# Kernel tuning notes

Measured on AMD Instinct MI355X. Metric: run time of the kernel, lower is better.

Reference implementation:

```python
import jax, jax.numpy as jnp
import numpy as np

B, S, D = 1, 2048, 6144
H, KV, HD = 48, 8, 128  # query heads, kv heads, head dim
THETA = 10000.0


def _rope_tables(seq_len, head_dim, theta):
    pos = jnp.arange(seq_len, dtype=jnp.float32)
    inv_freq = 1.0 / (theta ** (jnp.arange(0, head_dim, 2, dtype=jnp.float32) / head_dim))
    freqs = pos[:, None] * inv_freq[None, :]                 # [S, HD/2]
    emb = jnp.concatenate([freqs, freqs], axis=-1)           # [S, HD]
    return jnp.cos(emb), jnp.sin(emb)


def setup_inputs() -> dict:
    key = jax.random.key(0)
    k1, k2, k3 = jax.random.split(key, 3)
    hidden_states = jax.random.normal(k1, (B, S, D), dtype=jnp.float32) * 0.02
    w_qkv = jax.random.normal(k2, (D, (H + 2 * KV) * HD), dtype=jnp.float32) * 0.02
    w_out = jax.random.normal(k3, (H * HD, D), dtype=jnp.float32) * 0.02
    cos, sin = _rope_tables(S, HD, THETA)
    return {"hidden_states": hidden_states, "cos": cos, "sin": sin,
            "w_qkv": w_qkv, "w_out": w_out}


def _rotate_half(x):
    x1, x2 = jnp.split(x, 2, axis=-1)
    return jnp.concatenate([-x2, x1], axis=-1)


def reference(hidden_states, cos, sin, w_qkv, w_out):
    b, s, d = hidden_states.shape
    # fused QKV projection
    qkv = jnp.einsum('bsd,de->bse', hidden_states, w_qkv)
    q = qkv[..., : H * HD].reshape(b, s, H, HD)
    k = qkv[..., H * HD: (H + KV) * HD].reshape(b, s, KV, HD)
    v = qkv[..., (H + KV) * HD:].reshape(b, s, KV, HD)
    # rotary embedding (rotate-half form)
    c = cos[None, :, None, :]
    sn = sin[None, :, None, :]
    q = q * c + _rotate_half(q) * sn
    k = k * c + _rotate_half(k) * sn
    # GQA: expand kv heads to query heads
    rep = H // KV
    k = jnp.repeat(k, rep, axis=2)  # [b, s, H, HD]
    v = jnp.repeat(v, rep, axis=2)
    scale = 1.0 / jnp.sqrt(jnp.float32(HD))
    scores = jnp.einsum('bqhd,bkhd->bhqk', q, k) * scale     # [b,H,S,S]
    causal = jnp.tril(jnp.ones((s, s), dtype=bool))
    scores = jnp.where(causal[None, None], scores, jnp.float32(-1e30))
    attn = jax.nn.softmax(scores, axis=-1)
    out = jnp.einsum('bhqk,bkhd->bqhd', attn, v).reshape(b, s, H * HD)
    return jnp.einsum('bsd,de->bse', out, w_out)
```

## Files before the change

kernel.cpp:

```cpp
#include <hip/hip_runtime.h>


#define S_   2048
#define D_   6144
#define H_   48
#define KV_  8
#define HD_  128
#define NQK  8192
#define REP  6

typedef __attribute__((ext_vector_type(8)))  __bf16 bf16x8;
typedef __attribute__((ext_vector_type(4)))  __bf16 bf16x4;
typedef __attribute__((ext_vector_type(2)))  __bf16 bf16x2;
typedef __attribute__((ext_vector_type(4)))  float  f32x4;
typedef __attribute__((ext_vector_type(16))) float  f32x16;
typedef __attribute__((ext_vector_type(4)))  float  float4v;

__device__ __forceinline__ void gl_lds16(const void* g, void* l) {
  __builtin_amdgcn_global_load_lds(
      (const __attribute__((address_space(1))) void*)g,
      (__attribute__((address_space(3))) void*)l, 16, 0, 0);
}

__device__ __forceinline__ unsigned pack2(float a, float b) {
  union { bf16x2 v; unsigned u; } x;
  x.v[0] = (__bf16)a; x.v[1] = (__bf16)b;
  return x.u;
}

__global__ __launch_bounds__(256) void cvt_bf16(const float* __restrict__ in,
                                                __bf16* __restrict__ out, int n4) {
  int stride = gridDim.x * 256;
  for (int i = blockIdx.x * 256 + threadIdx.x; i < n4; i += stride) {
    float4v v = ((const float4v*)in)[i];
    bf16x4 o;
    o[0] = (__bf16)v[0]; o[1] = (__bf16)v[1];
    o[2] = (__bf16)v[2]; o[3] = (__bf16)v[3];
    ((bf16x4*)out)[i] = o;
  }
}

__global__ __launch_bounds__(256) void wtrans(const float* __restrict__ src,
                                              __bf16* __restrict__ dst,
                                              int K, int N) {
  __shared__ float t[32][33];
  const int n0 = blockIdx.x * 32, k0 = blockIdx.y * 32;
  const int tx = threadIdx.x, ty = threadIdx.y;
#pragma unroll
  for (int r = 0; r < 4; ++r)
    t[ty + r * 8][tx] = src[(size_t)(k0 + ty + r * 8) * N + n0 + tx];
  __syncthreads();
#pragma unroll
  for (int r = 0; r < 4; ++r)
    dst[(size_t)(n0 + ty + r * 8) * K + k0 + tx] = (__bf16)t[tx][ty + r * 8];
}

template <typename CT, int BN>
__global__ __launch_bounds__(512, 2) void gemm_bt(const __bf16* __restrict__ A,
                                                  const __bf16* __restrict__ BT,
                                                  CT* __restrict__ C,
                                                  int M, int N, int K) {
  constexpr int NB = BN / 64;
  constexpr int NF = BN / 64;
  __shared__ __align__(16) __bf16 As[2][256 * 64];
  __shared__ __align__(16) __bf16 Bs[2][BN * 64];
  const int tid = threadIdx.x;
  const int w = tid >> 6, l = tid & 63;
  const int lr = l & 15, lg = l >> 4;
  const int wm = w >> 2, wn = w & 3;
  const int nwg = gridDim.x * gridDim.y;
  int bid = blockIdx.y * gridDim.x + blockIdx.x;
  bid = (bid & 7) * (nwg >> 3) + (bid >> 3);
  const int m0 = (bid / gridDim.x) * 256, n0 = (bid % gridDim.x) * BN;
  const int nkt = K >> 6;

  auto stage_all = [&](int T) {
    const int buf = T & 1, k0 = T << 6;
#pragma unroll
    for (int j = 0; j < 4; ++j) {
      int idx = j * 512 + tid;
      int row = idx >> 3;
      int c = (idx & 7) ^ (row & 7);
      gl_lds16(A + (size_t)(m0 + row) * K + k0 + c * 8,
               As[buf] + (size_t)(j * 512 + w * 64) * 8);
    }
#pragma unroll
    for (int j = 0; j < NB; ++j) {
      int idx = j * 512 + tid;
      int row = idx >> 3;
      int c = (idx & 7) ^ (row & 7);
      gl_lds16(BT + (size_t)(n0 + row) * K + k0 + c * 8,
               Bs[buf] + (size_t)(j * 512 + w * 64) * 8);
    }
  };
  auto rdA = [&](const __bf16* Ab, int mh, int kk, bf16x8* afr) {
#pragma unroll
    for (int m = 0; m < 4; ++m) {
      int row = wm * 128 + (mh * 4 + m) * 16 + lr;
      afr[m] = *(const bf16x8*)(Ab + (size_t)row * 64
                                + (((kk * 4 + lg) ^ (lr & 7)) * 8));
    }
  };
  auto rdB = [&](const __bf16* Bb, int kk, bf16x8* bfr) {
#pragma unroll
    for (int n = 0; n < NF; ++n) {
      int row = wn * (BN / 4) + n * 16 + lr;
      bfr[n] = *(const bf16x8*)(Bb + (size_t)row * 64
                                + (((kk * 4 + lg) ^ (lr & 7)) * 8));
    }
  };
#define SBAR  __builtin_amdgcn_s_barrier()
#define MFMA_CLUSTER(ACC_OFF)                                                   \
  __builtin_amdgcn_s_setprio(1);                                               \
  _Pragma("unroll")                                                             \
  for (int m = 0; m < 4; ++m)                                                   \
    _Pragma("unroll")                                                           \
    for (int n = 0; n < NF; ++n)                                                \
      acc[(ACC_OFF) + m][n] = __builtin_amdgcn_mfma_f32_16x16x32_bf16(          \
          afr[m], bfr[n], acc[(ACC_OFF) + m][n], 0, 0, 0);                      \
  __builtin_amdgcn_s_setprio(0)

  f32x4 acc[8][NF] = {};
  stage_all(0);
  asm volatile("s_waitcnt vmcnt(0)" ::: "memory");
  SBAR;

  for (int T = 0; T < nkt; ++T) {
    const __bf16* Ab = As[T & 1];
    const __bf16* Bb = Bs[T & 1];
    bf16x8 afr[4], bfr[NF];
    rdA(Ab, 0, 0, afr);
    rdB(Bb, 0, bfr);
    if (T + 1 < nkt) stage_all(T + 1);
    MFMA_CLUSTER(0);
    SBAR;
    rdA(Ab, 1, 0, afr);
    MFMA_CLUSTER(4);
    SBAR;
    rdA(Ab, 0, 1, afr);
    rdB(Bb, 1, bfr);
    MFMA_CLUSTER(0);
    SBAR;
    rdA(Ab, 1, 1, afr);
    MFMA_CLUSTER(4);
    asm volatile("s_waitcnt lgkmcnt(0)" ::: "memory");
    if (T + 1 < nkt) asm volatile("s_waitcnt vmcnt(0)" ::: "memory");
    SBAR;
  }
#undef SBAR
#undef MFMA_CLUSTER
#pragma unroll
  for (int m = 0; m < 8; ++m)
#pragma unroll
    for (int n = 0; n < NF; ++n)
#pragma unroll
      for (int j = 0; j < 4; ++j) {
        int row = m0 + wm * 128 + m * 16 + lg * 4 + j;
        int col = n0 + wn * (BN / 4) + n * 16 + lr;
        C[(size_t)row * N + col] = (CT)acc[m][n][j];
      }
}

template <typename CT>
__global__ __launch_bounds__(256, 2) void gemm_bt128(const __bf16* __restrict__ A,
                                                     const __bf16* __restrict__ BT,
                                                     CT* __restrict__ C,
                                                     int M, int N, int K) {
  __shared__ __align__(16) __bf16 As[2][128 * 64];
  __shared__ __align__(16) __bf16 Bs[2][128 * 64];
  const int tid = threadIdx.x;
  const int w = tid >> 6, l = tid & 63;
  const int lr = l & 15, lg = l >> 4;
  const int wm = w >> 1, wn = w & 1;
  const int nwg = gridDim.x * gridDim.y;
  int bid = blockIdx.y * gridDim.x + blockIdx.x;
  bid = (bid & 7) * (nwg >> 3) + (bid >> 3);
  const int m0 = (bid / gridDim.x) * 128, n0 = (bid % gridDim.x) * 128;
  const int nkt = K >> 6;

  auto stage_all = [&](int T) {
    const int buf = T & 1, k0 = T << 6;
#pragma unroll
    for (int j = 0; j < 4; ++j) {
      int idx = j * 256 + tid;
      int row = idx >> 3;
      int c = (idx & 7) ^ (row & 7);
      gl_lds16(A + (size_t)(m0 + row) * K + k0 + c * 8,
               As[buf] + (size_t)(j * 256 + w * 64) * 8);
      gl_lds16(BT + (size_t)(n0 + row) * K + k0 + c * 8,
               Bs[buf] + (size_t)(j * 256 + w * 64) * 8);
    }
  };
  auto rd = [&](const __bf16* Sb, int rbase, int kk, bf16x8* fr) {
#pragma unroll
    for (int m = 0; m < 4; ++m) {
      int row = rbase + m * 16 + lr;
      fr[m] = *(const bf16x8*)(Sb + (size_t)row * 64
                               + (((kk * 4 + lg) ^ (lr & 7)) * 8));
    }
  };

  f32x4 acc[4][4] = {};
  stage_all(0);
  asm volatile("s_waitcnt vmcnt(0)" ::: "memory");
  __builtin_amdgcn_s_barrier();

  for (int T = 0; T < nkt; ++T) {
    const __bf16* Ab = As[T & 1];
    const __bf16* Bb = Bs[T & 1];
    bf16x8 afr[4], bfr[4];
    rd(Ab, wm * 64, 0, afr);
    rd(Bb, wn * 64, 0, bfr);
    if (T + 1 < nkt) stage_all(T + 1);
    __builtin_amdgcn_s_setprio(1);
#pragma unroll
    for (int m = 0; m < 4; ++m)
#pragma unroll
      for (int n = 0; n < 4; ++n)
        acc[m][n] = __builtin_amdgcn_mfma_f32_16x16x32_bf16(afr[m], bfr[n], acc[m][n], 0, 0, 0);
    __builtin_amdgcn_s_setprio(0);
    __builtin_amdgcn_s_barrier();
    rd(Ab, wm * 64, 1, afr);
    rd(Bb, wn * 64, 1, bfr);
    __builtin_amdgcn_s_setprio(1);
#pragma unroll
    for (int m = 0; m < 4; ++m)
#pragma unroll
      for (int n = 0; n < 4; ++n)
        acc[m][n] = __builtin_amdgcn_mfma_f32_16x16x32_bf16(afr[m], bfr[n], acc[m][n], 0, 0, 0);
    __builtin_amdgcn_s_setprio(0);
    asm volatile("s_waitcnt lgkmcnt(0)" ::: "memory");
    if (T + 1 < nkt) asm volatile("s_waitcnt vmcnt(0)" ::: "memory");
    __builtin_amdgcn_s_barrier();
  }
#pragma unroll
  for (int m = 0; m < 4; ++m)
#pragma unroll
    for (int n = 0; n < 4; ++n)
#pragma unroll
      for (int j = 0; j < 4; ++j) {
        int row = m0 + wm * 64 + m * 16 + lg * 4 + j;
        int col = n0 + wn * 64 + n * 16 + lr;
        C[(size_t)row * N + col] = (CT)acc[m][n][j];
      }
}

__global__ __launch_bounds__(256) void rope_qk(const __bf16* __restrict__ qkv,
                                               const float* __restrict__ cosT,
                                               const float* __restrict__ sinT,
                                               __bf16* __restrict__ Qo,
                                               __bf16* __restrict__ Ko) {
  const int s = blockIdx.x;
  const __bf16* base = qkv + (size_t)s * NQK;
  const float* ct = cosT + s * HD_;
  const float* st = sinT + s * HD_;
  const float scale = 0.1275174313f;
  for (int q4 = threadIdx.x; q4 < H_ * HD_ / 4; q4 += 256) {
    int h = q4 >> 5, d = (q4 & 31) * 4;
    bf16x4 x  = *(const bf16x4*)(base + h * HD_ + d);
    bf16x4 xr = (d < 64) ? *(const bf16x4*)(base + h * HD_ + d + 64)
                         : *(const bf16x4*)(base + h * HD_ + d - 64);
    float4v c4 = *(const float4v*)(ct + d);
    float4v s4 = *(const float4v*)(st + d);
    bf16x4 o;
#pragma unroll
    for (int j = 0; j < 4; ++j) {
      float r = (d < 64) ? -(float)xr[j] : (float)xr[j];
      o[j] = (__bf16)(((float)x[j] * c4[j] + r * s4[j]) * scale);
    }
    *(bf16x4*)(Qo + ((size_t)s * H_ + h) * HD_ + d) = o;
  }
  for (int q4 = threadIdx.x; q4 < KV_ * HD_ / 4; q4 += 256) {
    int h = q4 >> 5, d = (q4 & 31) * 4;
    const __bf16* kb = base + H_ * HD_;
    bf16x4 x  = *(const bf16x4*)(kb + h * HD_ + d);
    bf16x4 xr = (d < 64) ? *(const bf16x4*)(kb + h * HD_ + d + 64)
                         : *(const bf16x4*)(kb + h * HD_ + d - 64);
    float4v c4 = *(const float4v*)(ct + d);
    float4v s4 = *(const float4v*)(st + d);
    bf16x4 o;
#pragma unroll
    for (int j = 0; j < 4; ++j) {
      float r = (d < 64) ? -(float)xr[j] : (float)xr[j];
      o[j] = (__bf16)((float)x[j] * c4[j] + r * s4[j]);
    }
    *(bf16x4*)(Ko + ((size_t)s * KV_ + h) * HD_ + d) = o;
  }
}

__global__ __launch_bounds__(256) void v_trans(const __bf16* __restrict__ qkv,
                                               __bf16* __restrict__ Vt) {
  __shared__ __bf16 t[32][36];
  const int s0 = blockIdx.x * 32, d0 = blockIdx.y * 32, h = blockIdx.z;
  const int tx = threadIdx.x, ty = threadIdx.y;
  *(bf16x4*)&t[ty][tx * 4] =
      *(const bf16x4*)(qkv + (size_t)(s0 + ty) * NQK + (H_ + KV_) * HD_ + h * HD_ + d0 + tx * 4);
  __syncthreads();
  bf16x4 o;
#pragma unroll
  for (int j = 0; j < 4; ++j) o[j] = t[tx * 4 + j][ty];
  *(bf16x4*)(Vt + ((size_t)h * HD_ + d0 + ty) * S_ + s0 + tx * 4) = o;
}

__global__ __launch_bounds__(256, 2) void attn(const __bf16* __restrict__ Q,
                                               const __bf16* __restrict__ Kb,
                                               const __bf16* __restrict__ Vt,
                                               __bf16* __restrict__ O) {
  __shared__ __align__(16) __bf16 Ks[2][64 * 128];
  __shared__ __align__(16) __bf16 Vs[2][128 * 64];
  const int bx = gridDim.x - 1 - blockIdx.x;
  const int h = blockIdx.y, kvh = h / REP;
  const int tid = threadIdx.x, w = tid >> 6, l = tid & 63;
  const int c = l & 31, g = l >> 5;
  const int qb = bx * 128;
  const int qrow = qb + w * 32 + c;
  const int tmax_w = (qb + w * 32 + 31) >> 6;
  const int NT = (qb >> 6) + 2;

  auto stage = [&](int t) {
    const int buf = t & 1;
    const int kbase = t << 6;
#pragma unroll
    for (int j = 0; j < 4; ++j) {
      int idx = j * 256 + tid;
      int row = idx >> 4, cc = (idx & 15) ^ (row & 15);
      gl_lds16(Kb + ((size_t)(kbase + row) * KV_ + kvh) * HD_ + cc * 8,
               Ks[buf] + (size_t)(j * 256 + w * 64) * 8);
    }
#pragma unroll
    for (int j = 0; j < 4; ++j) {
      int idx = j * 256 + tid;
      int row = idx >> 3, cc = (idx & 7) ^ (row & 7);
      gl_lds16(Vt + (size_t)(kvh * HD_ + row) * S_ + kbase + cc * 8,
               Vs[buf] + (size_t)(j * 256 + w * 64) * 8);
    }
  };

  bf16x8 qf[8];
  const __bf16* qp = Q + ((size_t)qrow * H_ + h) * HD_ + g * 8;
#pragma unroll
  for (int st = 0; st < 8; ++st) qf[st] = *(const bf16x8*)(qp + st * 16);

  f32x16 o[4] = {};
  float m = -1e30f, lsum = 0.f;

  stage(0);
  __syncthreads();
  for (int t = 0; t < NT; ++t) {
    const int buf = t & 1;
    if (t + 1 < NT) stage(t + 1);
    if (t <= tmax_w) {
      const int kbase = t << 6;
      f32x16 s0 = {}, s1 = {};
      __builtin_amdgcn_s_setprio(1);
#pragma unroll
      for (int st = 0; st < 8; ++st) {
        int ch = ((st * 2 + g) ^ (c & 15)) * 8;
        bf16x8 k0 = *(const bf16x8*)(Ks[buf] + (size_t)c * 128 + ch);
        bf16x8 k1 = *(const bf16x8*)(Ks[buf] + (size_t)(32 + c) * 128 + ch);
        s0 = __builtin_amdgcn_mfma_f32_32x32x16_bf16(k0, qf[st], s0, 0, 0, 0);
        s1 = __builtin_amdgcn_mfma_f32_32x32x16_bf16(k1, qf[st], s1, 0, 0, 0);
      }
      __builtin_amdgcn_s_setprio(0);
      if (t == tmax_w) {
#pragma unroll
        for (int r = 0; r < 16; ++r) {
          int krow = (r & 3) + 8 * (r >> 2) + 4 * g;
          if (kbase + krow > qrow)      s0[r] = -1e30f;
          if (kbase + 32 + krow > qrow) s1[r] = -1e30f;
        }
      }
      float mj = s0[0];
#pragma unroll
      for (int r = 1; r < 16; ++r) mj = fmaxf(mj, s0[r]);
#pragma unroll
      for (int r = 0; r < 16; ++r) mj = fmaxf(mj, s1[r]);
      mj = fmaxf(mj, __shfl_xor(mj, 32));
      if (!__all(mj - m <= 8.0f)) {
        float mnew = fmaxf(m, mj);
        float sc = __builtin_amdgcn_exp2f(m - mnew);
        lsum *= sc;
#pragma unroll
        for (int db = 0; db < 4; ++db)
#pragma unroll
          for (int r = 0; r < 16; ++r) o[db][r] *= sc;
        m = mnew;
      }
      float rs = 0.f;
      float p0[16], p1[16];
#pragma unroll
      for (int r = 0; r < 16; ++r) { p0[r] = __builtin_amdgcn_exp2f(s0[r] - m); rs += p0[r]; }
#pragma unroll
      for (int r = 0; r < 16; ++r) { p1[r] = __builtin_amdgcn_exp2f(s1[r] - m); rs += p1[r]; }
      rs += __shfl_xor(rs, 32);
      lsum += rs;
      unsigned bq[4][4];
#pragma unroll
      for (int n = 0; n < 2; ++n)
#pragma unroll
        for (int tq = 0; tq < 2; ++tq) {
          const float* pp = n ? p1 : p0;
          unsigned q0 = pack2(pp[8 * tq + 0], pp[8 * tq + 1]);
          unsigned q1 = pack2(pp[8 * tq + 2], pp[8 * tq + 3]);
          unsigned q2 = pack2(pp[8 * tq + 4], pp[8 * tq + 5]);
          unsigned q3 = pack2(pp[8 * tq + 6], pp[8 * tq + 7]);
          unsigned v0 = g ? q0 : q2;
          unsigned v1 = g ? q1 : q3;
          unsigned sh0 = (unsigned)__shfl_xor((int)v0, 32);
          unsigned sh1 = (unsigned)__shfl_xor((int)v1, 32);
          int s = n * 2 + tq;
          bq[s][0] = g ? sh0 : q0;
          bq[s][1] = g ? sh1 : q1;
          bq[s][2] = g ? q2 : sh0;
          bq[s][3] = g ? q3 : sh1;
        }
      __builtin_amdgcn_s_setprio(1);
#pragma unroll
      for (int s = 0; s < 4; ++s) {
        union { unsigned u[4]; bf16x8 v; } bb;
        bb.u[0] = bq[s][0]; bb.u[1] = bq[s][1]; bb.u[2] = bq[s][2]; bb.u[3] = bq[s][3];
#pragma unroll
        for (int db = 0; db < 4; ++db) {
          int ch = ((s * 2 + g) ^ (c & 7)) * 8;
          bf16x8 vfr = *(const bf16x8*)(Vs[buf] + (size_t)(db * 32 + c) * 64 + ch);
          o[db] = __builtin_amdgcn_mfma_f32_32x32x16_bf16(vfr, bb.v, o[db], 0, 0, 0);
        }
      }
      __builtin_amdgcn_s_setprio(0);
    }
    if (t + 1 < NT) __syncthreads();
  }
  float inv = 1.f / lsum;
#pragma unroll
  for (int db = 0; db < 4; ++db)
#pragma unroll
    for (int rg = 0; rg < 4; ++rg) {
      bf16x4 ov;
#pragma unroll
      for (int j = 0; j < 4; ++j) ov[j] = (__bf16)(o[db][rg * 4 + j] * inv);
      *(bf16x4*)(O + (size_t)qrow * D_ + h * HD_ + db * 32 + rg * 8 + g * 4) = ov;
    }
}

extern "C" void kernel_launch(void* const* d_in, const int* in_sizes, int n_in,
                              void* d_out, int out_size, void* d_ws, size_t ws_size,
                              hipStream_t stream) {
  const float* hidden = (const float*)d_in[0];
  const float* cosT   = (const float*)d_in[1];
  const float* sinT   = (const float*)d_in[2];
  const float* w_qkv  = (const float*)d_in[3];
  const float* w_out  = (const float*)d_in[4];
  float* out = (float*)d_out;
  char* ws = (char*)d_ws;

  __bf16* wT   = (__bf16*)ws;
  __bf16* hb   = (__bf16*)(ws + 100663296);
  __bf16* qkvb = (__bf16*)(ws + 100663296 + 25165824);
  __bf16* q_b  = (__bf16*)(ws + 100663296 + 25165824 + 33554432);
  __bf16* k_b  = q_b + (size_t)S_ * H_ * HD_;
  __bf16* vt_b = k_b + (size_t)S_ * KV_ * HD_;

  cvt_bf16<<<dim3(2048), dim3(256), 0, stream>>>(hidden, hb, (int)((size_t)S_ * D_ / 4));
  wtrans<<<dim3(NQK / 32, D_ / 32), dim3(32, 8), 0, stream>>>(w_qkv, wT, D_, NQK);
  gemm_bt<__bf16, 256><<<dim3(NQK / 256, S_ / 256), dim3(512), 0, stream>>>(hb, wT, qkvb, S_, NQK, D_);
  rope_qk<<<dim3(S_), dim3(256), 0, stream>>>(qkvb, cosT, sinT, q_b, k_b);
  v_trans<<<dim3(S_ / 32, HD_ / 32, KV_), dim3(8, 32), 0, stream>>>(qkvb, vt_b);
  wtrans<<<dim3(D_ / 32, D_ / 32), dim3(32, 8), 0, stream>>>(w_out, wT, D_, D_);
  attn<<<dim3(S_ / 128, H_), dim3(256), 0, stream>>>(q_b, k_b, vt_b, hb);
  gemm_bt128<float><<<dim3(D_ / 128, S_ / 128), dim3(256), 0, stream>>>(hb, wT, out, S_, D_, D_);
}
```

Measured before the change: 678.7 us.

## Vectorize weight transpose, retile output GEMM to 128x192, simplify attention rescale

The weight transpose kernel now reads float4 rows and writes 8-wide bf16 vectors over 64x32 tiles. This cuts memory transactions in the fp32-to-bf16 weight conversion, which runs every call. The output projection GEMM moves to 512-thread blocks with 128x192 tiles, giving 512 workgroups and more waves per block. The attention kernel drops its lazy conditional rescale for an unconditional online-softmax rescale and no longer reverses block order. That removes the branch but adds 64 multiplies per iteration and may hurt load balance on the causal mask.

```diff
diff --git a/kernel.cpp b/kernel.cpp
--- a/kernel.cpp
+++ b/kernel.cpp
@@ -43,16 +43,24 @@
 __global__ __launch_bounds__(256) void wtrans(const float* __restrict__ src,
                                               __bf16* __restrict__ dst,
                                               int K, int N) {
-  __shared__ float t[32][33];
-  const int n0 = blockIdx.x * 32, k0 = blockIdx.y * 32;
-  const int tx = threadIdx.x, ty = threadIdx.y;
-#pragma unroll
-  for (int r = 0; r < 4; ++r)
-    t[ty + r * 8][tx] = src[(size_t)(k0 + ty + r * 8) * N + n0 + tx];
+  __shared__ float t[64][37];
+  const int n0 = blockIdx.x * 32, k0 = blockIdx.y * 64;
+  const int tid = threadIdx.x;
+  const int kr = tid >> 3, nc = (tid & 7) * 4;
+#pragma unroll
+  for (int i = 0; i < 2; ++i) {
+    float4v v = *(const float4v*)(src + (size_t)(k0 + kr + i * 32) * N + n0 + nc);
+    t[kr + i * 32][nc + 0] = v[0];
+    t[kr + i * 32][nc + 1] = v[1];
+    t[kr + i * 32][nc + 2] = v[2];
+    t[kr + i * 32][nc + 3] = v[3];
+  }
   __syncthreads();
-#pragma unroll
-  for (int r = 0; r < 4; ++r)
-    dst[(size_t)(n0 + ty + r * 8) * K + k0 + tx] = (__bf16)t[tx][ty + r * 8];
+  const int nr = tid >> 3, kc = (tid & 7) * 8;
+  bf16x8 o;
+#pragma unroll
+  for (int j = 0; j < 8; ++j) o[j] = (__bf16)t[kc + j][nr];
+  *(bf16x8*)(dst + (size_t)(n0 + nr) * K + k0 + kc) = o;
 }
 
 template <typename CT, int BN>
@@ -162,45 +170,59 @@
 }
 
 template <typename CT>
-__global__ __launch_bounds__(256, 2) void gemm_bt128(const __bf16* __restrict__ A,
-                                                     const __bf16* __restrict__ BT,
-                                                     CT* __restrict__ C,
-                                                     int M, int N, int K) {
+__global__ __launch_bounds__(512, 2) void gemm2_bt(const __bf16* __restrict__ A,
+                                                   const __bf16* __restrict__ BT,
+                                                   CT* __restrict__ C,
+                                                   int M, int N, int K) {
   __shared__ __align__(16) __bf16 As[2][128 * 64];
-  __shared__ __align__(16) __bf16 Bs[2][128 * 64];
+  __shared__ __align__(16) __bf16 Bs[2][192 * 64];
   const int tid = threadIdx.x;
   const int w = tid >> 6, l = tid & 63;
   const int lr = l & 15, lg = l >> 4;
-  const int wm = w >> 1, wn = w & 1;
+  const int wm = w >> 2, wn = w & 3;
   const int nwg = gridDim.x * gridDim.y;
   int bid = blockIdx.y * gridDim.x + blockIdx.x;
   bid = (bid & 7) * (nwg >> 3) + (bid >> 3);
-  const int m0 = (bid / gridDim.x) * 128, n0 = (bid % gridDim.x) * 128;
+  const int m0 = (bid / gridDim.x) * 128, n0 = (bid % gridDim.x) * 192;
   const int nkt = K >> 6;
 
   auto stage_all = [&](int T) {
     const int buf = T & 1, k0 = T << 6;
 #pragma unroll
-    for (int j = 0; j < 4; ++j) {
-      int idx = j * 256 + tid;
+    for (int j = 0; j < 2; ++j) {
+      int idx = j * 512 + tid;
       int row = idx >> 3;
       int c = (idx & 7) ^ (row & 7);
       gl_lds16(A + (size_t)(m0 + row) * K + k0 + c * 8,
-               As[buf] + (size_t)(j * 256 + w * 64) * 8);
+               As[buf] + (size_t)(j * 512 + w * 64) * 8);
+    }
+#pragma unroll
+    for (int j = 0; j < 3; ++j) {
+      int idx = j * 512 + tid;
+      int row = idx >> 3;
+      int c = (idx & 7) ^ (row & 7);
       gl_lds16(BT + (size_t)(n0 + row) * K + k0 + c * 8,
-               Bs[buf] + (size_t)(j * 256 + w * 64) * 8);
-    }
-  };
-  auto rd = [&](const __bf16* Sb, int rbase, int kk, bf16x8* fr) {
+               Bs[buf] + (size_t)(j * 512 + w * 64) * 8);
+    }
+  };
+  auto rdA = [&](const __bf16* Ab, int kk, bf16x8* afr) {
 #pragma unroll
     for (int m = 0; m < 4; ++m) {
-      int row = rbase + m * 16 + lr;
-      fr[m] = *(const bf16x8*)(Sb + (size_t)row * 64
-                               + (((kk * 4 + lg) ^ (lr & 7)) * 8));
-    }
-  };
-
-  f32x4 acc[4][4] = {};
+      int row = wm * 64 + m * 16 + lr;
+      afr[m] = *(const bf16x8*)(Ab + (size_t)row * 64
+                                + (((kk * 4 + lg) ^ (lr & 7)) * 8));
+    }
+  };
+  auto rdB = [&](const __bf16* Bb, int kk, bf16x8* bfr) {
+#pragma unroll
+    for (int n = 0; n < 3; ++n) {
+      int row = wn * 48 + n * 16 + lr;
+      bfr[n] = *(const bf16x8*)(Bb + (size_t)row * 64
+                                + (((kk * 4 + lg) ^ (lr & 7)) * 8));
+    }
+  };
+
+  f32x4 acc[4][3] = {};
   stage_all(0);
   asm volatile("s_waitcnt vmcnt(0)" ::: "memory");
   __builtin_amdgcn_s_barrier();
@@ -208,25 +230,25 @@
   for (int T = 0; T < nkt; ++T) {
     const __bf16* Ab = As[T & 1];
     const __bf16* Bb = Bs[T & 1];
-    bf16x8 afr[4], bfr[4];
-    rd(Ab, wm * 64, 0, afr);
-    rd(Bb, wn * 64, 0, bfr);
+    bf16x8 afr[4], bfr[3];
+    rdA(Ab, 0, afr);
+    rdB(Bb, 0, bfr);
     if (T + 1 < nkt) stage_all(T + 1);
     __builtin_amdgcn_s_setprio(1);
 #pragma unroll
     for (int m = 0; m < 4; ++m)
 #pragma unroll
-      for (int n = 0; n < 4; ++n)
+      for (int n = 0; n < 3; ++n)
         acc[m][n] = __builtin_amdgcn_mfma_f32_16x16x32_bf16(afr[m], bfr[n], acc[m][n], 0, 0, 0);
     __builtin_amdgcn_s_setprio(0);
     __builtin_amdgcn_s_barrier();
-    rd(Ab, wm * 64, 1, afr);
-    rd(Bb, wn * 64, 1, bfr);
+    rdA(Ab, 1, afr);
+    rdB(Bb, 1, bfr);
     __builtin_amdgcn_s_setprio(1);
 #pragma unroll
     for (int m = 0; m < 4; ++m)
 #pragma unroll
-      for (int n = 0; n < 4; ++n)
+      for (int n = 0; n < 3; ++n)
         acc[m][n] = __builtin_amdgcn_mfma_f32_16x16x32_bf16(afr[m], bfr[n], acc[m][n], 0, 0, 0);
     __builtin_amdgcn_s_setprio(0);
     asm volatile("s_waitcnt lgkmcnt(0)" ::: "memory");
@@ -236,11 +258,11 @@
 #pragma unroll
   for (int m = 0; m < 4; ++m)
 #pragma unroll
-    for (int n = 0; n < 4; ++n)
+    for (int n = 0; n < 3; ++n)
 #pragma unroll
       for (int j = 0; j < 4; ++j) {
         int row = m0 + wm * 64 + m * 16 + lg * 4 + j;
-        int col = n0 + wn * 64 + n * 16 + lr;
+        int col = n0 + wn * 48 + n * 16 + lr;
         C[(size_t)row * N + col] = (CT)acc[m][n][j];
       }
 }
@@ -308,8 +330,7 @@
                                                __bf16* __restrict__ O) {
   __shared__ __align__(16) __bf16 Ks[2][64 * 128];
   __shared__ __align__(16) __bf16 Vs[2][128 * 64];
-  const int bx = gridDim.x - 1 - blockIdx.x;
-  const int h = blockIdx.y, kvh = h / REP;
+  const int bx = blockIdx.x, h = blockIdx.y, kvh = h / REP;
   const int tid = threadIdx.x, w = tid >> 6, l = tid & 63;
   const int c = l & 31, g = l >> 5;
   const int qb = bx * 128;
@@ -376,24 +397,21 @@
 #pragma unroll
       for (int r = 0; r < 16; ++r) mj = fmaxf(mj, s1[r]);
       mj = fmaxf(mj, __shfl_xor(mj, 32));
-      if (!__all(mj - m <= 8.0f)) {
-        float mnew = fmaxf(m, mj);
-        float sc = __builtin_amdgcn_exp2f(m - mnew);
-        lsum *= sc;
-#pragma unroll
-        for (int db = 0; db < 4; ++db)
-#pragma unroll
-          for (int r = 0; r < 16; ++r) o[db][r] *= sc;
-        m = mnew;
-      }
+      float mnew = fmaxf(m, mj);
+      float sc = __builtin_amdgcn_exp2f(m - mnew);
       float rs = 0.f;
       float p0[16], p1[16];
 #pragma unroll
-      for (int r = 0; r < 16; ++r) { p0[r] = __builtin_amdgcn_exp2f(s0[r] - m); rs += p0[r]; }
-#pragma unroll
-      for (int r = 0; r < 16; ++r) { p1[r] = __builtin_amdgcn_exp2f(s1[r] - m); rs += p1[r]; }
+      for (int r = 0; r < 16; ++r) { p0[r] = __builtin_amdgcn_exp2f(s0[r] - mnew); rs += p0[r]; }
+#pragma unroll
+      for (int r = 0; r < 16; ++r) { p1[r] = __builtin_amdgcn_exp2f(s1[r] - mnew); rs += p1[r]; }
       rs += __shfl_xor(rs, 32);
-      lsum += rs;
+      lsum = lsum * sc + rs;
+      m = mnew;
+#pragma unroll
+      for (int db = 0; db < 4; ++db)
+#pragma unroll
+        for (int r = 0; r < 16; ++r) o[db][r] *= sc;
       unsigned bq[4][4];
 #pragma unroll
       for (int n = 0; n < 2; ++n)
@@ -461,11 +479,11 @@
   __bf16* vt_b = k_b + (size_t)S_ * KV_ * HD_;
 
   cvt_bf16<<<dim3(2048), dim3(256), 0, stream>>>(hidden, hb, (int)((size_t)S_ * D_ / 4));
-  wtrans<<<dim3(NQK / 32, D_ / 32), dim3(32, 8), 0, stream>>>(w_qkv, wT, D_, NQK);
+  wtrans<<<dim3(NQK / 32, D_ / 64), dim3(256), 0, stream>>>(w_qkv, wT, D_, NQK);
   gemm_bt<__bf16, 256><<<dim3(NQK / 256, S_ / 256), dim3(512), 0, stream>>>(hb, wT, qkvb, S_, NQK, D_);
   rope_qk<<<dim3(S_), dim3(256), 0, stream>>>(qkvb, cosT, sinT, q_b, k_b);
   v_trans<<<dim3(S_ / 32, HD_ / 32, KV_), dim3(8, 32), 0, stream>>>(qkvb, vt_b);
-  wtrans<<<dim3(D_ / 32, D_ / 32), dim3(32, 8), 0, stream>>>(w_out, wT, D_, D_);
+  wtrans<<<dim3(D_ / 32, D_ / 64), dim3(256), 0, stream>>>(w_out, wT, D_, D_);
   attn<<<dim3(S_ / 128, H_), dim3(256), 0, stream>>>(q_b, k_b, vt_b, hb);
-  gemm_bt128<float><<<dim3(D_ / 128, S_ / 128), dim3(256), 0, stream>>>(hb, wT, out, S_, D_, D_);
-}
+  gemm2_bt<float><<<dim3(D_ / 192, S_ / 128), dim3(512), 0, stream>>>(hb, wT, out, S_, D_, D_);
+}
```

After: 628.4 us. 1.08x faster.
